# Kernel optimization log

Measured on AMD Instinct MI355X. Metric: run time of the kernel, lower is better.

Reference implementation:

```python
import jax, jax.numpy as jnp
import numpy as np

N = 50000      # total nodes
E = 800000     # total edges
B = 512        # number of graphs (batch size)
D_IN, H, D_OUT = 5, 96, 192
EPS = 1e-5


def setup_inputs() -> dict:
    key = jax.random.key(0)
    ks = jax.random.split(key, 20)
    s = lambda d: 1.0 / np.sqrt(d)
    inp = {
        "x": jax.random.normal(ks[0], (N, D_IN), jnp.float32),
        "edge_index": jax.random.randint(ks[1], (2, E), 0, N, jnp.int64),
        "batch": jnp.sort(jax.random.randint(ks[2], (N,), 0, B, jnp.int64)),
        "W_in": jax.random.normal(ks[3], (D_IN, H), jnp.float32) * s(D_IN),
        "b_in": jnp.zeros((H,), jnp.float32),
        "W1": jax.random.normal(ks[4], (H, H), jnp.float32) * s(H),
        "b1": jnp.zeros((H,), jnp.float32),
        "g1": jnp.ones((H,), jnp.float32),
        "be1": jnp.zeros((H,), jnp.float32),
        "W2": jax.random.normal(ks[5], (H, H), jnp.float32) * s(H),
        "b2": jnp.zeros((H,), jnp.float32),
        "g2": jnp.ones((H,), jnp.float32),
        "be2": jnp.zeros((H,), jnp.float32),
        "W_out": jax.random.normal(ks[6], (H, D_OUT), jnp.float32) * s(H),
        "b_out": jnp.zeros((D_OUT,), jnp.float32),
        "ln_g": jnp.ones((D_OUT,), jnp.float32),
        "ln_b": jnp.zeros((D_OUT,), jnp.float32),
    }
    return inp


def gcn_conv(h, W, b, src, dst):
    # PyG GCNConv: h' = D^{-1/2} (A + I) D^{-1/2} (h W) + b, deg from self-looped graph
    h = h @ W                                           # [N, H]
    deg = jnp.ones((N,), h.dtype).at[dst].add(jnp.ones((E,), h.dtype))
    dinv = jax.lax.rsqrt(deg)                           # [N]
    coef = dinv[src] * dinv[dst]                        # [E]
    agg = jnp.zeros_like(h).at[dst].add(h[src] * coef[:, None])
    agg = agg + h * (dinv * dinv)[:, None]              # self-loop term
    return agg + b


def batch_norm(x, g, b):
    m = x.mean(0)
    v = x.var(0)
    return g * (x - m) * jax.lax.rsqrt(v + EPS) + b


def reference(x, edge_index, batch, W_in, b_in, W1, b1, g1, be1, W2, b2, g2, be2,
              W_out, b_out, ln_g, ln_b):
    src, dst = edge_index[0], edge_index[1]
    h = jax.nn.relu(x @ W_in + b_in)
    for (W, bb, g, be) in ((W1, b1, g1, be1), (W2, b2, g2, be2)):
        r = h
        h = gcn_conv(h, W, bb, src, dst)
        h = jax.nn.relu(batch_norm(h, g, be))           # dropout = identity (eval)
        h = h + r
    counts = jnp.zeros((B,), h.dtype).at[batch].add(1.0)
    pooled = jax.ops.segment_sum(h, batch, num_segments=B)
    pooled = pooled / jnp.maximum(counts, 1.0)[:, None]  # global_mean_pool [B, H]
    out = pooled @ W_out + b_out                         # [B, D_OUT]
    mu = out.mean(-1, keepdims=True)
    var = out.var(-1, keepdims=True)
    return ln_g * (out - mu) * jax.lax.rsqrt(var + EPS) + ln_b
```

## Files before the change

### kernel.cpp

```cpp
#include <hip/hip_runtime.h>
#include <hip/hip_bf16.h>
#include <stdint.h>

#define NN 50000
#define EE 800000
#define BB 512
#define HH 96
#define DIN 5
#define DOUT 192
#define EPSV 1e-5f
#define NBANK 32
#define NB_GATHER 3125
#define NBLK_SCAN ((NN + 1023) / 1024)
#define NBUK 512
#define BUKN 98
#define FILLB 128
#define FCHUNK (EE / FILLB)

__device__ inline float blo(uint32_t w) { return __uint_as_float(w << 16); }
__device__ inline float bhi(uint32_t w) { return __uint_as_float(w & 0xffff0000u); }
__device__ inline uint32_t packbf(float a, float b) {
    uint32_t ua = __float_as_uint(a); ua += 0x7fffu + ((ua >> 16) & 1u);
    uint32_t ub = __float_as_uint(b); ub += 0x7fffu + ((ub >> 16) & 1u);
    return (ua >> 16) | (ub & 0xffff0000u);
}

__global__ void k_deghist(const int* __restrict__ dst, int* __restrict__ degi) {
    int e = blockIdx.x * blockDim.x + threadIdx.x;
    if (e < EE) atomicAdd(&degi[dst[e]], 1);
}

__global__ __launch_bounds__(1024) void k_scan1(const int* __restrict__ degi,
                                                int* __restrict__ row_ptr,
                                                int* __restrict__ bsum,
                                                float* __restrict__ dinv,
                                                int* __restrict__ histg) {
    __shared__ int wsum[16], woff[16];
    __shared__ int dh[64];
    int tid = threadIdx.x;
    if (tid < 64) dh[tid] = 0;
    __syncthreads();
    int i = blockIdx.x * 1024 + tid;
    int v = (i < NN) ? degi[i] : 0;
    if (i < NN) {
        dinv[i] = rsqrtf((float)v + 1.0f);
        atomicAdd(&dh[min(v, 63)], 1);
    }
    int lane = tid & 63, w = tid >> 6;
    int x = v;
#pragma unroll
    for (int o = 1; o < 64; o <<= 1) {
        int y = __shfl_up(x, o, 64);
        if (lane >= o) x += y;
    }
    if (lane == 63) wsum[w] = x;
    __syncthreads();
    if (tid == 0) {
        int c = 0;
#pragma unroll
        for (int k = 0; k < 16; ++k) { woff[k] = c; c += wsum[k]; }
        bsum[blockIdx.x] = c;
    }
    __syncthreads();
    if (i < NN) row_ptr[i] = woff[w] + x - v;
    if (tid < 64) histg[blockIdx.x * 64 + tid] = dh[tid];
}

__global__ __launch_bounds__(256) void k_scan2(int* __restrict__ bsum,
                                               int* __restrict__ row_ptr,
                                               float* __restrict__ stats,
                                               int* __restrict__ histg) {
    __shared__ int tot[64], binbase[64];
    int t = threadIdx.x;
    for (int i = t; i < 2 * NBANK * 192; i += 256) stats[i] = 0.0f;
    if (t == 0) {
        int c = 0;
        for (int k = 0; k < NBLK_SCAN; ++k) { int s = bsum[k]; bsum[k] = c; c += s; }
        row_ptr[NN] = c;
    }
    if (t < 64) {
        int s = 0;
        for (int k = 0; k < NBLK_SCAN; ++k) s += histg[k * 64 + t];
        tot[t] = s;
    }
    __syncthreads();
    if (t == 1) {
        int c = 0;
        for (int b = 0; b < 64; ++b) { binbase[b] = c; c += tot[b]; }
    }
    __syncthreads();
    if (t < 64) {
        int c = binbase[t];
        for (int k = 0; k < NBLK_SCAN; ++k) {
            int tmp = histg[k * 64 + t];
            histg[k * 64 + t] = c;
            c += tmp;
        }
    }
}

__global__ __launch_bounds__(1024) void k_scan3(const int* __restrict__ bsum,
                                                int* __restrict__ row_ptr,
                                                int* __restrict__ bcur) {
    int i = blockIdx.x * 1024 + threadIdx.x;
    if (i < NN) {
        int rp = row_ptr[i] + bsum[blockIdx.x];
        row_ptr[i] = rp;
        if (i % BUKN == 0) bcur[i / BUKN] = rp;
    }
}

__global__ __launch_bounds__(1024) void k_dperm(const int* __restrict__ degi,
                                                const int* __restrict__ histg,
                                                int* __restrict__ perm) {
    __shared__ int lcur[64];
    int tid = threadIdx.x;
    if (tid < 64) lcur[tid] = histg[blockIdx.x * 64 + tid];
    __syncthreads();
    int i = blockIdx.x * 1024 + tid;
    if (i < NN) {
        int pos = atomicAdd(&lcur[min(degi[i], 63)], 1);
        perm[pos] = i;
    }
}

__global__ __launch_bounds__(256) void k_bucket(const int* __restrict__ src,
                                                const int* __restrict__ dst,
                                                int* __restrict__ bcur,
                                                uint32_t* __restrict__ ebuf) {
    __shared__ int hist[NBUK], bbase[NBUK], cnt[NBUK];
    int tid = threadIdx.x;
    int e0 = blockIdx.x * FCHUNK, e1 = e0 + FCHUNK;
    for (int j = tid; j < NBUK; j += 256) { hist[j] = 0; cnt[j] = 0; }
    __syncthreads();
    for (int e = e0 + tid; e < e1; e += 256) atomicAdd(&hist[dst[e] / BUKN], 1);
    __syncthreads();
    for (int j = tid; j < NBUK; j += 256) bbase[j] = atomicAdd(&bcur[j], hist[j]);
    __syncthreads();
    for (int e = e0 + tid; e < e1; e += 256) {
        int d = dst[e];
        int b = d / BUKN;
        int off = atomicAdd(&cnt[b], 1);
        ebuf[bbase[b] + off] = (uint32_t)src[e] | ((uint32_t)(d - b * BUKN) << 16);
    }
}

__global__ __launch_bounds__(256) void k_fill2(const uint32_t* __restrict__ ebuf,
                                               const int* __restrict__ row_ptr,
                                               int* __restrict__ col) {
    __shared__ int lrp[BUKN], lcur[BUKN];
    int b = blockIdx.x, tid = threadIdx.x;
    int node0 = b * BUKN;
    if (node0 >= NN) return;
    int node1 = min(node0 + BUKN, NN);
    int nn = node1 - node0;
    for (int j = tid; j < nn; j += 256) { lrp[j] = row_ptr[node0 + j]; lcur[j] = 0; }
    __syncthreads();
    int ebase = row_ptr[node0], eend = row_ptr[node1];
    for (int i = ebase + tid; i < eend; i += 256) {
        uint32_t w = ebuf[i];
        int drel = (int)(w >> 16);
        int off = atomicAdd(&lcur[drel], 1);
        col[lrp[drel] + off] = (int)(w & 0xffffu);
    }
}

__device__ inline void store48(uint32_t* __restrict__ hwb, int gr, int q,
                               const float* acc, float dval) {
    uint32_t wv[12];
#pragma unroll
    for (int p = 0; p < 12; ++p) wv[p] = packbf(acc[2 * p] * dval, acc[2 * p + 1] * dval);
    uint4* dstp = reinterpret_cast<uint4*>(&hwb[(size_t)gr * 48 + q * 12]);
    dstp[0] = make_uint4(wv[0], wv[1], wv[2], wv[3]);
    dstp[1] = make_uint4(wv[4], wv[5], wv[6], wv[7]);
    dstp[2] = make_uint4(wv[8], wv[9], wv[10], wv[11]);
}

__global__ __launch_bounds__(256) void k_gemm_in(const float* __restrict__ x,
                                                 const float* __restrict__ Win,
                                                 const float* __restrict__ bin,
                                                 const float* __restrict__ W1,
                                                 const float* __restrict__ dinv,
                                                 float* __restrict__ h0,
                                                 uint32_t* __restrict__ hwb) {
    __shared__ float sA[64][100];
    __shared__ float sW[96 * 96];
    __shared__ float sWin[5 * 96];
    __shared__ float sbin[96];
    int tid = threadIdx.x;
    int row0 = blockIdx.x * 64;

    for (int i = tid; i < 96 * 96; i += 256) sW[i] = W1[i];
    for (int i = tid; i < 5 * 96; i += 256) sWin[i] = Win[i];
    if (tid < 96) sbin[tid] = bin[tid];
    __syncthreads();

    int r = tid >> 2, q = tid & 3;
    int j0 = q * 24;
    int gr = row0 + r;

    {
        float xv[5];
#pragma unroll
        for (int k = 0; k < DIN; ++k) xv[k] = (gr < NN) ? x[gr * DIN + k] : 0.0f;
        float hv[24];
#pragma unroll
        for (int jj = 0; jj < 24; ++jj) {
            float acc = sbin[j0 + jj];
#pragma unroll
            for (int k = 0; k < DIN; ++k) acc += xv[k] * sWin[k * 96 + j0 + jj];
            hv[jj] = fmaxf(acc, 0.0f);
            sA[r][j0 + jj] = hv[jj];
        }
        if (gr < NN) {
#pragma unroll
            for (int jj = 0; jj < 24; jj += 4)
                *reinterpret_cast<float4*>(&h0[(size_t)gr * 96 + j0 + jj]) =
                    make_float4(hv[jj], hv[jj + 1], hv[jj + 2], hv[jj + 3]);
        }
    }
    __syncthreads();

    float acc[24];
#pragma unroll
    for (int jj = 0; jj < 24; ++jj) acc[jj] = 0.0f;
    for (int k = 0; k < 96; ++k) {
        float a = sA[r][k];
#pragma unroll
        for (int jj = 0; jj < 24; ++jj) acc[jj] += a * sW[k * 96 + j0 + jj];
    }
    if (gr < NN) store48(hwb, gr, q, acc, dinv[gr]);
}

__global__ __launch_bounds__(256) void k_gather(const uint32_t* __restrict__ hwb,
                                                const float* __restrict__ dinv,
                                                const int* __restrict__ row_ptr,
                                                const int* __restrict__ col,
                                                const int* __restrict__ perm,
                                                float* __restrict__ agg,
                                                float* __restrict__ stats) {
    int tid = threadIdx.x;
    int t = tid & 15, slot = tid >> 4;
    int n = perm[blockIdx.x * 16 + slot];

    size_t rn = (size_t)n * 48;
    uint32_t w0 = hwb[rn + t], w1 = hwb[rn + 16 + t], w2 = hwb[rn + 32 + t];
    float a0 = blo(w0), a1 = bhi(w0);
    float a2 = blo(w1), a3 = bhi(w1);
    float a4 = blo(w2), a5 = bhi(w2);

    int beg = row_ptr[n], end = row_ptr[n + 1];
    int p = beg;
    for (; p + 3 < end; p += 4) {
        int s0 = col[p], s1 = col[p + 1], s2 = col[p + 2], s3 = col[p + 3];
        size_t r0 = (size_t)s0 * 48, r1 = (size_t)s1 * 48;
        size_t r2 = (size_t)s2 * 48, r3 = (size_t)s3 * 48;
        uint32_t u00 = hwb[r0 + t], u01 = hwb[r0 + 16 + t], u02 = hwb[r0 + 32 + t];
        uint32_t u10 = hwb[r1 + t], u11 = hwb[r1 + 16 + t], u12 = hwb[r1 + 32 + t];
        uint32_t u20 = hwb[r2 + t], u21 = hwb[r2 + 16 + t], u22 = hwb[r2 + 32 + t];
        uint32_t u30 = hwb[r3 + t], u31 = hwb[r3 + 16 + t], u32 = hwb[r3 + 32 + t];
        a0 += blo(u00); a1 += bhi(u00); a2 += blo(u01); a3 += bhi(u01);
        a4 += blo(u02); a5 += bhi(u02);
        a0 += blo(u10); a1 += bhi(u10); a2 += blo(u11); a3 += bhi(u11);
        a4 += blo(u12); a5 += bhi(u12);
        a0 += blo(u20); a1 += bhi(u20); a2 += blo(u21); a3 += bhi(u21);
        a4 += blo(u22); a5 += bhi(u22);
        a0 += blo(u30); a1 += bhi(u30); a2 += blo(u31); a3 += bhi(u31);
        a4 += blo(u32); a5 += bhi(u32);
    }
    for (; p < end; ++p) {
        size_t rs = (size_t)col[p] * 48;
        uint32_t u0 = hwb[rs + t], u1 = hwb[rs + 16 + t], u2 = hwb[rs + 32 + t];
        a0 += blo(u0); a1 += bhi(u0);
        a2 += blo(u1); a3 += bhi(u1);
        a4 += blo(u2); a5 += bhi(u2);
    }
    float dn = dinv[n];
    a0 *= dn; a1 *= dn; a2 *= dn; a3 *= dn; a4 *= dn; a5 *= dn;

    float* an = agg + (size_t)n * 96;
    *reinterpret_cast<float2*>(&an[2 * t])      = make_float2(a0, a1);
    *reinterpret_cast<float2*>(&an[2 * t + 32]) = make_float2(a2, a3);
    *reinterpret_cast<float2*>(&an[2 * t + 64]) = make_float2(a4, a5);

    __shared__ float red[2][96];
    if (tid < 96) { red[0][tid] = 0.0f; red[1][tid] = 0.0f; }
    __syncthreads();
    int c0 = 2 * t;
    int colsv[6] = {c0, c0 + 1, c0 + 32, c0 + 33, c0 + 64, c0 + 65};
    float cs[6] = {a0, a1, a2, a3, a4, a5};
#pragma unroll
    for (int k = 0; k < 6; ++k) {
        atomicAdd(&red[0][colsv[k]], cs[k]);
        atomicAdd(&red[1][colsv[k]], cs[k] * cs[k]);
    }
    __syncthreads();
    float* bank = stats + (blockIdx.x & (NBANK - 1)) * 192;
    if (tid < 96) {
        atomicAdd(&bank[tid], red[0][tid]);
        atomicAdd(&bank[96 + tid], red[1][tid]);
    }
}

__global__ __launch_bounds__(256) void k_gemm_bn(const float* __restrict__ agg,
                                                 const float* __restrict__ hprev,
                                                 const float* __restrict__ stats,
                                                 const float* __restrict__ g,
                                                 const float* __restrict__ be,
                                                 const float* __restrict__ W,
                                                 const float* __restrict__ dinv,
                                                 float* __restrict__ hnew,
                                                 uint32_t* __restrict__ hwb) {
    __shared__ float sA[64][100];
    __shared__ float sW[96 * 96];
    __shared__ float ssc[96], ssh[96];
    int tid = threadIdx.x;
    int row0 = blockIdx.x * 64;

    for (int i = tid; i < 96 * 96; i += 256) sW[i] = W[i];
    if (tid < 96) {
        float s = 0.0f, s2 = 0.0f;
#pragma unroll
        for (int k = 0; k < NBANK; ++k) { s += stats[k * 192 + tid]; s2 += stats[k * 192 + 96 + tid]; }
        float m = s * (1.0f / NN);
        float var = s2 * (1.0f / NN) - m * m;
        float sc = g[tid] * rsqrtf(var + EPSV);
        ssc[tid] = sc;
        ssh[tid] = be[tid] - m * sc;
    }
    __syncthreads();

    for (int i = tid; i < 64 * 24; i += 256) {
        int r = i / 24, qq = i % 24;
        int gr = row0 + r, c = qq * 4;
        float4 v = make_float4(0.0f, 0.0f, 0.0f, 0.0f);
        if (gr < NN) {
            float4 a = *reinterpret_cast<const float4*>(&agg[(size_t)gr * 96 + c]);
            float4 pv = *reinterpret_cast<const float4*>(&hprev[(size_t)gr * 96 + c]);
            v.x = fmaxf(a.x * ssc[c]     + ssh[c],     0.0f) + pv.x;
            v.y = fmaxf(a.y * ssc[c + 1] + ssh[c + 1], 0.0f) + pv.y;
            v.z = fmaxf(a.z * ssc[c + 2] + ssh[c + 2], 0.0f) + pv.z;
            v.w = fmaxf(a.w * ssc[c + 3] + ssh[c + 3], 0.0f) + pv.w;
            *reinterpret_cast<float4*>(&hnew[(size_t)gr * 96 + c]) = v;
        }
        *reinterpret_cast<float4*>(&sA[r][c]) = v;
    }
    __syncthreads();

    int r = tid >> 2, q = tid & 3;
    int j0 = q * 24;
    int gr = row0 + r;
    float acc[24];
#pragma unroll
    for (int jj = 0; jj < 24; ++jj) acc[jj] = 0.0f;
    for (int k = 0; k < 96; ++k) {
        float a = sA[r][k];
#pragma unroll
        for (int jj = 0; jj < 24; ++jj) acc[jj] += a * sW[k * 96 + j0 + jj];
    }
    if (gr < NN) store48(hwb, gr, q, acc, dinv[gr]);
}

__device__ inline int lower_bound_i(const int* __restrict__ a, int n, int v) {
    int lo = 0, hi = n;
    while (lo < hi) { int mid = (lo + hi) >> 1; if (a[mid] < v) lo = mid + 1; else hi = mid; }
    return lo;
}

__global__ __launch_bounds__(192) void k_out(const float* __restrict__ agg,
                                             const float* __restrict__ hprev,
                                             const float* __restrict__ stats,
                                             const float* __restrict__ g,
                                             const float* __restrict__ be,
                                             const int* __restrict__ batch,
                                             const float* __restrict__ Wout,
                                             const float* __restrict__ bout,
                                             const float* __restrict__ lg,
                                             const float* __restrict__ lb,
                                             float* __restrict__ out) {
    __shared__ float ssc[96], ssh[96];
    __shared__ float sp2[2][96];
    __shared__ float sp[96];
    int b = blockIdx.x, t = threadIdx.x;
    if (t < 96) {
        float s = 0.0f, s2 = 0.0f;
#pragma unroll
        for (int k = 0; k < NBANK; ++k) { s += stats[k * 192 + t]; s2 += stats[k * 192 + 96 + t]; }
        float m = s * (1.0f / NN);
        float var = s2 * (1.0f / NN) - m * m;
        float sc = g[t] * rsqrtf(var + EPSV);
        ssc[t] = sc;
        ssh[t] = be[t] - m * sc;
    }
    int lo = lower_bound_i(batch, NN, b);
    int hi = lower_bound_i(batch, NN, b + 1);
    __syncthreads();

    int colc = t % 96, half = t / 96;
    float scc = ssc[colc], shc = ssh[colc];
    float accp = 0.0f;
    for (int r = lo + half; r < hi; r += 2) {
        size_t idx = (size_t)r * 96 + colc;
        accp += fmaxf(agg[idx] * scc + shc, 0.0f) + hprev[idx];
    }
    sp2[half][colc] = accp;
    __syncthreads();
    if (t < 96) {
        float inv = (hi > lo) ? 1.0f / (float)(hi - lo) : 0.0f;
        sp[t] = (sp2[0][t] + sp2[1][t]) * inv;
    }
    __syncthreads();

    float acc = bout[t];
    for (int k = 0; k < 96; ++k) acc += sp[k] * Wout[k * 192 + t];

    __shared__ float svals[192];
    __shared__ float smv[2];
    svals[t] = acc;
    __syncthreads();
    if (t < 64) {
        float a0 = svals[t], a1 = svals[t + 64], a2 = svals[t + 128];
        float s = a0 + a1 + a2;
        float s2 = a0 * a0 + a1 * a1 + a2 * a2;
        for (int o = 32; o > 0; o >>= 1) {
            s += __shfl_down(s, o, 64);
            s2 += __shfl_down(s2, o, 64);
        }
        if (t == 0) { smv[0] = s * (1.0f / 192.0f); smv[1] = s2 * (1.0f / 192.0f); }
    }
    __syncthreads();
    float m = smv[0];
    float var = smv[1] - m * m;
    float rr = rsqrtf(var + EPSV);
    out[b * 192 + t] = lg[t] * (acc - m) * rr + lb[t];
}

extern "C" void kernel_launch(void* const* d_in, const int* in_sizes, int n_in,
                              void* d_out, int out_size, void* d_ws, size_t ws_size,
                              hipStream_t stream) {
    const float* x    = (const float*)d_in[0];
    const int*   ei   = (const int*)  d_in[1];
    const int*   batch= (const int*)  d_in[2];
    const float* Win  = (const float*)d_in[3];
    const float* bin  = (const float*)d_in[4];
    const float* W1   = (const float*)d_in[5];
    const float* g1   = (const float*)d_in[7];
    const float* be1  = (const float*)d_in[8];
    const float* W2   = (const float*)d_in[9];
    const float* g2   = (const float*)d_in[11];
    const float* be2  = (const float*)d_in[12];
    const float* Wout = (const float*)d_in[13];
    const float* bout = (const float*)d_in[14];
    const float* lg   = (const float*)d_in[15];
    const float* lb   = (const float*)d_in[16];
    const int* src = ei;
    const int* dst = ei + EE;

    float*    ws_f   = (float*)d_ws;
    float*    h0     = ws_f;
    float*    h1     = h0 + (size_t)NN * HH;
    float*    agg    = h1 + (size_t)NN * HH;
    float*    dinv   = agg + (size_t)NN * HH;
    float*    stats  = dinv + NN;
    uint32_t* hwb    = (uint32_t*)(stats + 2 * NBANK * 192);
    int*      degi   = (int*)(hwb + (size_t)NN * 48);
    int*      histg  = degi + NN;
    int*      row_ptr= histg + NBLK_SCAN * 64;
    int*      perm   = row_ptr + NN + 1;
    int*      bsum   = perm + NN;
    int*      bcur   = bsum + NBLK_SCAN;
    int*      col    = bcur + NBUK;
    uint32_t* ebuf   = (uint32_t*)agg;

    const int TB = 256;
    float* stats1 = stats;
    float* stats2 = stats + NBANK * 192;

    hipMemsetAsync(degi, 0, NN * sizeof(int), stream);
    k_deghist<<<(EE + TB - 1) / TB, TB, 0, stream>>>(dst, degi);
    k_scan1<<<NBLK_SCAN, 1024, 0, stream>>>(degi, row_ptr, bsum, dinv, histg);
    k_scan2<<<1, 256, 0, stream>>>(bsum, row_ptr, stats, histg);
    k_scan3<<<NBLK_SCAN, 1024, 0, stream>>>(bsum, row_ptr, bcur);
    k_dperm<<<NBLK_SCAN, 1024, 0, stream>>>(degi, histg, perm);
    k_bucket<<<FILLB, TB, 0, stream>>>(src, dst, bcur, ebuf);
    k_fill2<<<NBUK, TB, 0, stream>>>(ebuf, row_ptr, col);

    k_gemm_in<<<(NN + 63) / 64, TB, 0, stream>>>(x, Win, bin, W1, dinv, h0, hwb);
    k_gather<<<NB_GATHER, TB, 0, stream>>>(hwb, dinv, row_ptr, col, perm, agg, stats1);

    k_gemm_bn<<<(NN + 63) / 64, TB, 0, stream>>>(agg, h0, stats1, g1, be1, W2, dinv, h1, hwb);
    k_gather<<<NB_GATHER, TB, 0, stream>>>(hwb, dinv, row_ptr, col, perm, agg, stats2);

    k_out<<<BB, 192, 0, stream>>>(agg, h1, stats2, g2, be2, batch, Wout, bout, lg, lb,
                                  (float*)d_out);
}
```

Measured before the change: 308.3 us.

## Build CSR via bucket histogram instead of global per-node degree atomics

Replaces the global per-edge degree atomic histogram and the multi-kernel node-level scan with a coarse bucket histogram, a single-block bucket scan, and bucket scatter. Each bucket block then derives per-node degrees, row_ptr, dinv and col locally in shared memory. This removes 800K global atomics and a full-node scan pass. The cost is an extra pass over ebuf per bucket and separate degree-histogram kernels for the degree-sorted permutation.

New measurement: 289.3 us. -6.1%, faster.

```diff
diff --git a/kernel.cpp b/kernel.cpp
--- a/kernel.cpp
+++ b/kernel.cpp
@@ -25,109 +25,43 @@
     return (ua >> 16) | (ub & 0xffff0000u);
 }
 
-__global__ void k_deghist(const int* __restrict__ dst, int* __restrict__ degi) {
-    int e = blockIdx.x * blockDim.x + threadIdx.x;
-    if (e < EE) atomicAdd(&degi[dst[e]], 1);
-}
-
-__global__ __launch_bounds__(1024) void k_scan1(const int* __restrict__ degi,
-                                                int* __restrict__ row_ptr,
-                                                int* __restrict__ bsum,
-                                                float* __restrict__ dinv,
-                                                int* __restrict__ histg) {
-    __shared__ int wsum[16], woff[16];
-    __shared__ int dh[64];
-    int tid = threadIdx.x;
-    if (tid < 64) dh[tid] = 0;
-    __syncthreads();
-    int i = blockIdx.x * 1024 + tid;
-    int v = (i < NN) ? degi[i] : 0;
-    if (i < NN) {
-        dinv[i] = rsqrtf((float)v + 1.0f);
-        atomicAdd(&dh[min(v, 63)], 1);
-    }
-    int lane = tid & 63, w = tid >> 6;
-    int x = v;
-#pragma unroll
-    for (int o = 1; o < 64; o <<= 1) {
-        int y = __shfl_up(x, o, 64);
-        if (lane >= o) x += y;
-    }
-    if (lane == 63) wsum[w] = x;
-    __syncthreads();
-    if (tid == 0) {
-        int c = 0;
-#pragma unroll
-        for (int k = 0; k < 16; ++k) { woff[k] = c; c += wsum[k]; }
-        bsum[blockIdx.x] = c;
-    }
-    __syncthreads();
-    if (i < NN) row_ptr[i] = woff[w] + x - v;
-    if (tid < 64) histg[blockIdx.x * 64 + tid] = dh[tid];
-}
-
-__global__ __launch_bounds__(256) void k_scan2(int* __restrict__ bsum,
-                                               int* __restrict__ row_ptr,
+__global__ __launch_bounds__(256) void k_bhist(const int* __restrict__ dst,
+                                               int* __restrict__ bkcnt) {
+    __shared__ int hist[NBUK];
+    int tid = threadIdx.x;
+    for (int j = tid; j < NBUK; j += 256) hist[j] = 0;
+    __syncthreads();
+    int e0 = blockIdx.x * FCHUNK;
+    for (int e = e0 + tid; e < e0 + FCHUNK; e += 256) atomicAdd(&hist[dst[e] / BUKN], 1);
+    __syncthreads();
+    for (int j = tid; j < NBUK; j += 256) if (hist[j]) atomicAdd(&bkcnt[j], hist[j]);
+}
+
+__global__ __launch_bounds__(256) void k_bscan(const int* __restrict__ bkcnt,
+                                               int* __restrict__ bkbase,
+                                               int* __restrict__ bkcur,
                                                float* __restrict__ stats,
-                                               int* __restrict__ histg) {
-    __shared__ int tot[64], binbase[64];
+                                               int* __restrict__ row_ptr) {
+    __shared__ int sc[NBUK + 1];
     int t = threadIdx.x;
     for (int i = t; i < 2 * NBANK * 192; i += 256) stats[i] = 0.0f;
+    for (int j = t; j < NBUK; j += 256) sc[j] = bkcnt[j];
+    __syncthreads();
     if (t == 0) {
         int c = 0;
-        for (int k = 0; k < NBLK_SCAN; ++k) { int s = bsum[k]; bsum[k] = c; c += s; }
+        for (int j = 0; j < NBUK; ++j) { int s = sc[j]; sc[j] = c; c += s; }
+        sc[NBUK] = c;
         row_ptr[NN] = c;
     }
-    if (t < 64) {
-        int s = 0;
-        for (int k = 0; k < NBLK_SCAN; ++k) s += histg[k * 64 + t];
-        tot[t] = s;
-    }
-    __syncthreads();
-    if (t == 1) {
-        int c = 0;
-        for (int b = 0; b < 64; ++b) { binbase[b] = c; c += tot[b]; }
-    }
-    __syncthreads();
-    if (t < 64) {
-        int c = binbase[t];
-        for (int k = 0; k < NBLK_SCAN; ++k) {
-            int tmp = histg[k * 64 + t];
-            histg[k * 64 + t] = c;
-            c += tmp;
-        }
-    }
-}
-
-__global__ __launch_bounds__(1024) void k_scan3(const int* __restrict__ bsum,
-                                                int* __restrict__ row_ptr,
-                                                int* __restrict__ bcur) {
-    int i = blockIdx.x * 1024 + threadIdx.x;
-    if (i < NN) {
-        int rp = row_ptr[i] + bsum[blockIdx.x];
-        row_ptr[i] = rp;
-        if (i % BUKN == 0) bcur[i / BUKN] = rp;
-    }
-}
-
-__global__ __launch_bounds__(1024) void k_dperm(const int* __restrict__ degi,
-                                                const int* __restrict__ histg,
-                                                int* __restrict__ perm) {
-    __shared__ int lcur[64];
-    int tid = threadIdx.x;
-    if (tid < 64) lcur[tid] = histg[blockIdx.x * 64 + tid];
-    __syncthreads();
-    int i = blockIdx.x * 1024 + tid;
-    if (i < NN) {
-        int pos = atomicAdd(&lcur[min(degi[i], 63)], 1);
-        perm[pos] = i;
-    }
-}
-
-__global__ __launch_bounds__(256) void k_bucket(const int* __restrict__ src,
-                                                const int* __restrict__ dst,
-                                                int* __restrict__ bcur,
-                                                uint32_t* __restrict__ ebuf) {
+    __syncthreads();
+    for (int j = t; j <= NBUK; j += 256) bkbase[j] = sc[j];
+    for (int j = t; j < NBUK; j += 256) bkcur[j] = sc[j];
+}
+
+__global__ __launch_bounds__(256) void k_bscat(const int* __restrict__ src,
+                                               const int* __restrict__ dst,
+                                               int* __restrict__ bkcur,
+                                               uint32_t* __restrict__ ebuf) {
     __shared__ int hist[NBUK], bbase[NBUK], cnt[NBUK];
     int tid = threadIdx.x;
     int e0 = blockIdx.x * FCHUNK, e1 = e0 + FCHUNK;
@@ -135,7 +69,7 @@
     __syncthreads();
     for (int e = e0 + tid; e < e1; e += 256) atomicAdd(&hist[dst[e] / BUKN], 1);
     __syncthreads();
-    for (int j = tid; j < NBUK; j += 256) bbase[j] = atomicAdd(&bcur[j], hist[j]);
+    for (int j = tid; j < NBUK; j += 256) bbase[j] = hist[j] ? atomicAdd(&bkcur[j], hist[j]) : 0;
     __syncthreads();
     for (int e = e0 + tid; e < e1; e += 256) {
         int d = dst[e];
@@ -145,23 +79,83 @@
     }
 }
 
-__global__ __launch_bounds__(256) void k_fill2(const uint32_t* __restrict__ ebuf,
-                                               const int* __restrict__ row_ptr,
-                                               int* __restrict__ col) {
-    __shared__ int lrp[BUKN], lcur[BUKN];
+__global__ __launch_bounds__(256) void k_csr(const uint32_t* __restrict__ ebuf,
+                                             const int* __restrict__ bkbase,
+                                             int* __restrict__ row_ptr,
+                                             int* __restrict__ col,
+                                             int* __restrict__ degi,
+                                             float* __restrict__ dinv) {
+    __shared__ int cnt[BUKN], base[BUKN], lcur[BUKN];
     int b = blockIdx.x, tid = threadIdx.x;
     int node0 = b * BUKN;
     if (node0 >= NN) return;
-    int node1 = min(node0 + BUKN, NN);
-    int nn = node1 - node0;
-    for (int j = tid; j < nn; j += 256) { lrp[j] = row_ptr[node0 + j]; lcur[j] = 0; }
-    __syncthreads();
-    int ebase = row_ptr[node0], eend = row_ptr[node1];
+    int nn = min(BUKN, NN - node0);
+    int ebase = bkbase[b], eend = bkbase[b + 1];
+    for (int j = tid; j < nn; j += 256) { cnt[j] = 0; lcur[j] = 0; }
+    __syncthreads();
+    for (int i = ebase + tid; i < eend; i += 256) atomicAdd(&cnt[ebuf[i] >> 16], 1);
+    __syncthreads();
+    if (tid == 0) {
+        int c = 0;
+        for (int j = 0; j < nn; ++j) { base[j] = c; c += cnt[j]; }
+    }
+    __syncthreads();
+    for (int j = tid; j < nn; j += 256) {
+        row_ptr[node0 + j] = ebase + base[j];
+        degi[node0 + j] = cnt[j];
+        dinv[node0 + j] = rsqrtf((float)cnt[j] + 1.0f);
+    }
     for (int i = ebase + tid; i < eend; i += 256) {
         uint32_t w = ebuf[i];
-        int drel = (int)(w >> 16);
-        int off = atomicAdd(&lcur[drel], 1);
-        col[lrp[drel] + off] = (int)(w & 0xffffu);
+        int dr = (int)(w >> 16);
+        int off = atomicAdd(&lcur[dr], 1);
+        col[ebase + base[dr] + off] = (int)(w & 0xffffu);
+    }
+}
+
+__global__ __launch_bounds__(1024) void k_dhist(const int* __restrict__ degi,
+                                                int* __restrict__ histg) {
+    __shared__ int dh[64];
+    int tid = threadIdx.x;
+    if (tid < 64) dh[tid] = 0;
+    __syncthreads();
+    int i = blockIdx.x * 1024 + tid;
+    if (i < NN) atomicAdd(&dh[min(degi[i], 63)], 1);
+    __syncthreads();
+    if (tid < 64) histg[blockIdx.x * 64 + tid] = dh[tid];
+}
+
+__global__ __launch_bounds__(64) void k_dscan(int* __restrict__ histg) {
+    __shared__ int tot[64], binbase[64];
+    int t = threadIdx.x;
+    int s = 0;
+    for (int k = 0; k < NBLK_SCAN; ++k) s += histg[k * 64 + t];
+    tot[t] = s;
+    __syncthreads();
+    if (t == 0) {
+        int c = 0;
+        for (int b2 = 0; b2 < 64; ++b2) { binbase[b2] = c; c += tot[b2]; }
+    }
+    __syncthreads();
+    int c = binbase[t];
+    for (int k = 0; k < NBLK_SCAN; ++k) {
+        int tmp = histg[k * 64 + t];
+        histg[k * 64 + t] = c;
+        c += tmp;
+    }
+}
+
+__global__ __launch_bounds__(1024) void k_dperm(const int* __restrict__ degi,
+                                                const int* __restrict__ histg,
+                                                int* __restrict__ perm) {
+    __shared__ int lcur[64];
+    int tid = threadIdx.x;
+    if (tid < 64) lcur[tid] = histg[blockIdx.x * 64 + tid];
+    __syncthreads();
+    int i = blockIdx.x * 1024 + tid;
+    if (i < NN) {
+        int pos = atomicAdd(&lcur[min(degi[i], 63)], 1);
+        perm[pos] = i;
     }
 }
 
@@ -467,23 +461,24 @@
     int*      histg  = degi + NN;
     int*      row_ptr= histg + NBLK_SCAN * 64;
     int*      perm   = row_ptr + NN + 1;
-    int*      bsum   = perm + NN;
-    int*      bcur   = bsum + NBLK_SCAN;
-    int*      col    = bcur + NBUK;
+    int*      bkcnt  = perm + NN;
+    int*      bkbase = bkcnt + NBUK;
+    int*      bkcur  = bkbase + NBUK + 1;
+    int*      col    = bkcur + NBUK;
     uint32_t* ebuf   = (uint32_t*)agg;
 
     const int TB = 256;
     float* stats1 = stats;
     float* stats2 = stats + NBANK * 192;
 
-    hipMemsetAsync(degi, 0, NN * sizeof(int), stream);
-    k_deghist<<<(EE + TB - 1) / TB, TB, 0, stream>>>(dst, degi);
-    k_scan1<<<NBLK_SCAN, 1024, 0, stream>>>(degi, row_ptr, bsum, dinv, histg);
-    k_scan2<<<1, 256, 0, stream>>>(bsum, row_ptr, stats, histg);
-    k_scan3<<<NBLK_SCAN, 1024, 0, stream>>>(bsum, row_ptr, bcur);
+    hipMemsetAsync(bkcnt, 0, NBUK * sizeof(int), stream);
+    k_bhist<<<FILLB, TB, 0, stream>>>(dst, bkcnt);
+    k_bscan<<<1, TB, 0, stream>>>(bkcnt, bkbase, bkcur, stats, row_ptr);
+    k_bscat<<<FILLB, TB, 0, stream>>>(src, dst, bkcur, ebuf);
+    k_csr<<<NBUK, TB, 0, stream>>>(ebuf, bkbase, row_ptr, col, degi, dinv);
+    k_dhist<<<NBLK_SCAN, 1024, 0, stream>>>(degi, histg);
+    k_dscan<<<1, 64, 0, stream>>>(histg);
     k_dperm<<<NBLK_SCAN, 1024, 0, stream>>>(degi, histg, perm);
-    k_bucket<<<FILLB, TB, 0, stream>>>(src, dst, bcur, ebuf);
-    k_fill2<<<NBUK, TB, 0, stream>>>(ebuf, row_ptr, col);
 
     k_gemm_in<<<(NN + 63) / 64, TB, 0, stream>>>(x, Win, bin, W1, dinv, h0, hwb);
     k_gather<<<NB_GATHER, TB, 0, stream>>>(hwb, dinv, row_ptr, col, perm, agg, stats1);
```
